# Kernel optimization log

Hardware: AMD Instinct MI355X
Metric: run time of the kernel (lower is better)

Reference implementation:

```python
import jax, jax.numpy as jnp
import numpy as np

B, N, C = 4, 2048, 1024
H = 16
D = C // H  # head_size = 64


def setup_inputs() -> dict:
    key = jax.random.key(0)
    ks = jax.random.split(key, 9)
    s = 1.0 / np.sqrt(C)
    return {
        "x": jax.random.normal(ks[0], (B, N, C), dtype=jnp.float32),
        "Wq": jax.random.normal(ks[1], (C, C), dtype=jnp.float32) * s,
        "bq": jnp.zeros((C,), dtype=jnp.float32),
        "Wk": jax.random.normal(ks[2], (C, C), dtype=jnp.float32) * s,
        "bk": jnp.zeros((C,), dtype=jnp.float32),
        "Wv": jax.random.normal(ks[3], (C, C), dtype=jnp.float32) * s,
        "bv": jnp.zeros((C,), dtype=jnp.float32),
        "Wo": jax.random.normal(ks[4], (C, C), dtype=jnp.float32) * s,
        "bo": jnp.zeros((C,), dtype=jnp.float32),
    }


def reference(x, Wq, bq, Wk, bk, Wv, bv, Wo, bo):
    scale = 1.0 / np.sqrt(D).astype(np.float32)
    # projections: [B,N,C] -> [B,H,N,D]
    def split_heads(t):
        return t.reshape(B, N, H, D).transpose(0, 2, 1, 3)
    q = split_heads(x @ Wq + bq)
    k = split_heads(x @ Wk + bk)
    v = split_heads(x @ Wv + bv)
    # scores: [B,H,N,N] -- full NxN materialized as in the original module
    attn = jnp.einsum("bhqd,bhkd->bhqk", q, k) * scale
    attn = jax.nn.softmax(attn, axis=-1)
    # context: [B,H,N,D] -> [B,N,C]
    ctx = jnp.einsum("bhqk,bhkd->bhqd", attn, v)
    ctx = ctx.transpose(0, 2, 1, 3).reshape(B, N, C)
    return ctx @ Wo + bo
```

## Files before the change

### kernel.cpp

```cpp
#include <hip/hip_runtime.h>
#include <hip/hip_bf16.h>

typedef __bf16 bf16_t;
typedef __bf16 bf16x4 __attribute__((ext_vector_type(4)));
typedef __bf16 bf16x8 __attribute__((ext_vector_type(8)));
typedef float f32x4 __attribute__((ext_vector_type(4)));
typedef unsigned int u32;

#define B_ 4
#define N_ 2048
#define C_ 1024
#define H_ 16
#define D_ 64

#define MFMA32(a, b, c) __builtin_amdgcn_mfma_f32_16x16x32_bf16((a), (b), (c), 0, 0, 0)

#if __has_builtin(__builtin_amdgcn_exp2f)
#define EXP2F(x) __builtin_amdgcn_exp2f(x)
#else
#define EXP2F(x) __expf((x) * 0.6931471805599453f)
#endif

#define QSCALE 0.18033688011112042f

__device__ __forceinline__ void async16(const bf16_t* g, bf16_t* l) {
    __builtin_amdgcn_global_load_lds(
        (const u32 __attribute__((address_space(1)))*)g,
        (u32 __attribute__((address_space(3)))*)l, 16, 0, 0);
}

__global__ __launch_bounds__(256)
void xconv_kernel(const float* __restrict__ x, bf16_t* __restrict__ xb)
{
    const size_t i = ((size_t)blockIdx.x * 256 + threadIdx.x) * 8;
    float4 a = *(const float4*)(x + i);
    float4 b = *(const float4*)(x + i + 4);
    bf16x8 o;
    o[0] = (bf16_t)a.x; o[1] = (bf16_t)a.y; o[2] = (bf16_t)a.z; o[3] = (bf16_t)a.w;
    o[4] = (bf16_t)b.x; o[5] = (bf16_t)b.y; o[6] = (bf16_t)b.z; o[7] = (bf16_t)b.w;
    *(bf16x8*)(xb + i) = o;
}

__global__ __launch_bounds__(256)
void wtrans_kernel(const float* __restrict__ W0, const float* __restrict__ W1,
                   const float* __restrict__ W2, const float* __restrict__ W3,
                   bf16_t* __restrict__ T0, bf16_t* __restrict__ T1,
                   bf16_t* __restrict__ T2, bf16_t* __restrict__ T3)
{
    const float* W; bf16_t* T;
    switch (blockIdx.z) {
        case 0:  W = W0; T = T0; break;
        case 1:  W = W1; T = T1; break;
        case 2:  W = W2; T = T2; break;
        default: W = W3; T = T3; break;
    }
    __shared__ bf16_t tile[64 * 72];
    const int tid = threadIdx.x;
    const int r0 = blockIdx.y * 64;
    const int c0 = blockIdx.x * 64;

    const int rr = tid >> 4;
    const int cc = (tid & 15) * 4;
    #pragma unroll
    for (int i = 0; i < 4; ++i) {
        const int row = rr + i * 16;
        float4 v = *(const float4*)(W + (size_t)(r0 + row) * C_ + c0 + cc);
        tile[(cc + 0) * 72 + row] = (bf16_t)v.x;
        tile[(cc + 1) * 72 + row] = (bf16_t)v.y;
        tile[(cc + 2) * 72 + row] = (bf16_t)v.z;
        tile[(cc + 3) * 72 + row] = (bf16_t)v.w;
    }
    __syncthreads();
    #pragma unroll
    for (int i = 0; i < 2; ++i) {
        const int ch = i * 256 + tid;
        const int n  = ch >> 3;
        const int k8 = (ch & 7) * 8;
        bf16x8 o = *(const bf16x8*)&tile[n * 72 + k8];
        *(bf16x8*)(T + (size_t)(c0 + n) * C_ + r0 + k8) = o;
    }
}

__global__ __launch_bounds__(256)
void gemm_qkv_kernel(const bf16_t* __restrict__ A, const bf16_t* __restrict__ Wt,
                     const float* __restrict__ bq, const float* __restrict__ bk,
                     const float* __restrict__ bv,
                     bf16_t* __restrict__ Qb, bf16_t* __restrict__ Kb,
                     bf16_t* __restrict__ Vtb)
{
    __shared__ bf16_t As[2][128 * 32];
    __shared__ bf16_t Bs[2][128 * 32];

    const int tid  = threadIdx.x;
    const int w    = tid >> 6;
    const int lane = tid & 63;
    const int c    = lane & 15;
    const int quad = lane >> 4;
    const int n0   = blockIdx.x * 128;
    const int m0   = blockIdx.y * 128;
    const int wm   = (w & 1) * 64;
    const int wn   = (w >> 1) * 64;

    f32x4 acc[4][4] = {};

    for (int k0 = 0; k0 < C_; k0 += 64) {
        __syncthreads();
        #pragma unroll
        for (int hh = 0; hh < 2; ++hh) {
            #pragma unroll
            for (int ph = 0; ph < 2; ++ph) {
                const int ch  = ph * 256 + tid;
                const int row = ch >> 2;
                const int k8  = (ch & 3) * 8;
                const int wbase = (ph * 256 + w * 64) * 8;
                async16(A  + (size_t)(m0 + row) * C_ + k0 + hh * 32 + k8, &As[hh][wbase]);
                async16(Wt + (size_t)(n0 + row) * C_ + k0 + hh * 32 + k8, &Bs[hh][wbase]);
            }
        }
        __syncthreads();

        bf16x8 af[2][4], bfr[2][4];
        #pragma unroll
        for (int hh = 0; hh < 2; ++hh) {
            #pragma unroll
            for (int mf = 0; mf < 4; ++mf)
                af[hh][mf] = *(const bf16x8*)&As[hh][(wm + mf * 16 + c) * 32 + quad * 8];
            #pragma unroll
            for (int nf = 0; nf < 4; ++nf)
                bfr[hh][nf] = *(const bf16x8*)&Bs[hh][(wn + nf * 16 + c) * 32 + quad * 8];
        }

        #pragma unroll
        for (int mf = 0; mf < 4; ++mf)
            #pragma unroll
            for (int nf = 0; nf < 4; ++nf) {
                acc[mf][nf] = MFMA32(af[0][mf], bfr[0][nf], acc[mf][nf]);
                acc[mf][nf] = MFMA32(af[1][mf], bfr[1][nf], acc[mf][nf]);
            }
    }

    const int which = n0 >> 10;
    const float* bias = (which == 0) ? bq : (which == 1) ? bk : bv;

    #pragma unroll
    for (int nf = 0; nf < 4; ++nf) {
        const int col  = n0 + wn + nf * 16 + c;
        const int ncol = col & 1023;
        const float bsf = bias[ncol];
        const int h = ncol >> 6, d = ncol & 63;
        #pragma unroll
        for (int mf = 0; mf < 4; ++mf) {
            const int rbase = m0 + wm + mf * 16 + quad * 4;
            if (which < 2) {
                bf16_t* out = which ? Kb : Qb;
                const float sc = which ? 1.0f : QSCALE;
                #pragma unroll
                for (int r = 0; r < 4; ++r) {
                    const int row = rbase + r;
                    const int bb = row >> 11, n = row & 2047;
                    out[(((size_t)bb * H_ + h) * N_ + n) * D_ + d] =
                        (bf16_t)((acc[mf][nf][r] + bsf) * sc);
                }
            } else {
                const int bb = rbase >> 11, nb = rbase & 2047;
                bf16x4 o;
                #pragma unroll
                for (int r = 0; r < 4; ++r) o[r] = (bf16_t)(acc[mf][nf][r] + bsf);
                *(bf16x4*)(Vtb + (((size_t)bb * H_ + h) * D_ + d) * N_ + nb) = o;
            }
        }
    }
}

__global__ __launch_bounds__(256)
void gemm_out_kernel(const bf16_t* __restrict__ A, const bf16_t* __restrict__ Bt,
                     const float* __restrict__ bias, float* __restrict__ out)
{
    __shared__ bf16_t As[2][128 * 32];
    __shared__ bf16_t Bs[2][128 * 32];

    const int tid  = threadIdx.x;
    const int w    = tid >> 6;
    const int lane = tid & 63;
    const int c    = lane & 15;
    const int quad = lane >> 4;
    const int n0   = blockIdx.x * 128;
    const int m0   = blockIdx.y * 128;
    const int wm   = (w & 1) * 64;
    const int wn   = (w >> 1) * 64;

    f32x4 acc[4][4] = {};

    for (int k0 = 0; k0 < C_; k0 += 64) {
        __syncthreads();
        #pragma unroll
        for (int hh = 0; hh < 2; ++hh) {
            #pragma unroll
            for (int ph = 0; ph < 2; ++ph) {
                const int ch  = ph * 256 + tid;
                const int row = ch >> 2;
                const int k8  = (ch & 3) * 8;
                const int wbase = (ph * 256 + w * 64) * 8;
                async16(A  + (size_t)(m0 + row) * C_ + k0 + hh * 32 + k8, &As[hh][wbase]);
                async16(Bt + (size_t)(n0 + row) * C_ + k0 + hh * 32 + k8, &Bs[hh][wbase]);
            }
        }
        __syncthreads();

        bf16x8 af[2][4], bfr[2][4];
        #pragma unroll
        for (int hh = 0; hh < 2; ++hh) {
            #pragma unroll
            for (int mf = 0; mf < 4; ++mf)
                af[hh][mf] = *(const bf16x8*)&As[hh][(wm + mf * 16 + c) * 32 + quad * 8];
            #pragma unroll
            for (int nf = 0; nf < 4; ++nf)
                bfr[hh][nf] = *(const bf16x8*)&Bs[hh][(wn + nf * 16 + c) * 32 + quad * 8];
        }

        #pragma unroll
        for (int mf = 0; mf < 4; ++mf)
            #pragma unroll
            for (int nf = 0; nf < 4; ++nf) {
                acc[mf][nf] = MFMA32(af[0][mf], bfr[0][nf], acc[mf][nf]);
                acc[mf][nf] = MFMA32(af[1][mf], bfr[1][nf], acc[mf][nf]);
            }
    }

    #pragma unroll
    for (int nf = 0; nf < 4; ++nf) {
        const int col   = n0 + wn + nf * 16 + c;
        const float bsf = bias[col];
        #pragma unroll
        for (int mf = 0; mf < 4; ++mf) {
            const int rbase = m0 + wm + mf * 16 + quad * 4;
            #pragma unroll
            for (int r = 0; r < 4; ++r)
                out[(size_t)(rbase + r) * C_ + col] = acc[mf][nf][r] + bsf;
        }
    }
}

__global__ __launch_bounds__(256, 2)
void attn_kernel(const bf16_t* __restrict__ Q, const bf16_t* __restrict__ K,
                 const bf16_t* __restrict__ Vt, bf16_t* __restrict__ ctx)
{
    __shared__ bf16_t ksh[64 * 64];
    __shared__ bf16_t vsh[64 * 64];

    const int tid  = threadIdx.x;
    const int w    = tid >> 6;
    const int lane = tid & 63;
    const int c    = lane & 15;
    const int quad = lane >> 4;

    const int bid   = blockIdx.x;
    const int bh    = (bid & 7) * 8 + ((bid >> 3) & 7);
    const int qtile = bid >> 6;
    const int b = bh >> 4, h = bh & 15;
    const size_t base = (size_t)bh * N_ * D_;
    const int qb = qtile * 256 + w * 64;

    bf16x8 qf[4][2];
    #pragma unroll
    for (int g = 0; g < 4; ++g)
        #pragma unroll
        for (int hh = 0; hh < 2; ++hh)
            qf[g][hh] = *(const bf16x8*)(Q + base + (size_t)(qb + g * 16 + c) * D_ + hh * 32 + quad * 8);

    bf16x8 ones;
    #pragma unroll
    for (int j = 0; j < 8; ++j) ones[j] = (bf16_t)1.0f;

    f32x4 O[4][4] = {};
    f32x4 O5[4] = {};

    for (int kt = 0; kt < N_; kt += 64) {
        __syncthreads();
        #pragma unroll
        for (int ph = 0; ph < 2; ++ph) {
            const int ch = ph * 256 + tid;
            const int rr = ch >> 3;
            const int e8 = ch & 7;
            const int sw = (e8 ^ (rr & 7)) * 8;
            bf16x8 kv = *(const bf16x8*)(K  + base + (size_t)(kt + rr) * D_ + e8 * 8);
            *(bf16x8*)&ksh[rr * 64 + sw] = kv;
            bf16x8 vv = *(const bf16x8*)(Vt + base + (size_t)rr * N_ + kt + e8 * 8);
            *(bf16x8*)&vsh[rr * 64 + sw] = vv;
        }
        __syncthreads();

        #pragma unroll
        for (int ss = 0; ss < 2; ++ss) {
            bf16x8 kb[2][2];
            #pragma unroll
            for (int s2 = 0; s2 < 2; ++s2) {
                const int key = (ss * 2 + s2) * 16 + c;
                #pragma unroll
                for (int hh = 0; hh < 2; ++hh)
                    kb[s2][hh] = *(const bf16x8*)&ksh[key * 64 + (((hh * 4 + quad) ^ (c & 7)) * 8)];
            }
            bf16x8 va[4];
            const int k8lo = ss * 4 + (quad >> 1);
            const int half = (quad & 1) * 4;
            #pragma unroll
            for (int df = 0; df < 4; ++df) {
                const int row = (df * 16 + c) * 64;
                bf16x4 lo = *(const bf16x4*)&vsh[row + ((k8lo       ^ (c & 7)) * 8) + half];
                bf16x4 hi = *(const bf16x4*)&vsh[row + (((k8lo + 2) ^ (c & 7)) * 8) + half];
                #pragma unroll
                for (int j = 0; j < 4; ++j) { va[df][j] = lo[j]; va[df][4 + j] = hi[j]; }
            }

            #pragma unroll
            for (int g = 0; g < 4; ++g) {
                f32x4 s0 = {}, s1 = {};
                s0 = MFMA32(kb[0][0], qf[g][0], s0);
                s0 = MFMA32(kb[0][1], qf[g][1], s0);
                s1 = MFMA32(kb[1][0], qf[g][0], s1);
                s1 = MFMA32(kb[1][1], qf[g][1], s1);

                bf16x8 pb;
                #pragma unroll
                for (int r = 0; r < 4; ++r) {
                    pb[r]     = (bf16_t)EXP2F(s0[r]);
                    pb[4 + r] = (bf16_t)EXP2F(s1[r]);
                }

                #pragma unroll
                for (int df = 0; df < 4; ++df)
                    O[g][df] = MFMA32(va[df], pb, O[g][df]);
                O5[g] = MFMA32(ones, pb, O5[g]);
            }
        }
    }

    #pragma unroll
    for (int g = 0; g < 4; ++g) {
        const float inv_l = 1.0f / O5[g][0];
        const int q = qb + g * 16 + c;
        #pragma unroll
        for (int df = 0; df < 4; ++df) {
            bf16x4 o;
            #pragma unroll
            for (int r = 0; r < 4; ++r) o[r] = (bf16_t)(O[g][df][r] * inv_l);
            *(bf16x4*)(ctx + ((size_t)b * N_ + q) * C_ + h * 64 + df * 16 + quad * 4) = o;
        }
    }
}

extern "C" void kernel_launch(void* const* d_in, const int* in_sizes, int n_in,
                              void* d_out, int out_size, void* d_ws, size_t ws_size,
                              hipStream_t stream) {
    const float* x  = (const float*)d_in[0];
    const float* Wq = (const float*)d_in[1];
    const float* bq = (const float*)d_in[2];
    const float* Wk = (const float*)d_in[3];
    const float* bk = (const float*)d_in[4];
    const float* Wv = (const float*)d_in[5];
    const float* bv = (const float*)d_in[6];
    const float* Wo = (const float*)d_in[7];
    const float* bo = (const float*)d_in[8];

    bf16_t* ws = (bf16_t*)d_ws;
    const size_t per = (size_t)B_ * N_ * C_;
    bf16_t* xb  = ws;
    bf16_t* ctx = ws;
    bf16_t* Qb  = ws + per;
    bf16_t* Kb  = ws + 2 * per;
    bf16_t* Vtb = ws + 3 * per;
    bf16_t* Wtqkv = ws + 4 * per;
    bf16_t* Wtq = Wtqkv;
    bf16_t* Wtk = Wtqkv + (size_t)C_ * C_;
    bf16_t* Wtv = Wtqkv + 2 * (size_t)C_ * C_;
    bf16_t* Wto = Wtqkv + 3 * (size_t)C_ * C_;

    dim3 blk(256);

    xconv_kernel<<<dim3(per / 2048), blk, 0, stream>>>(x, xb);
    wtrans_kernel<<<dim3(16, 16, 4), blk, 0, stream>>>(Wq, Wk, Wv, Wo, Wtq, Wtk, Wtv, Wto);

    gemm_qkv_kernel<<<dim3(24, 64), blk, 0, stream>>>(xb, Wtqkv, bq, bk, bv, Qb, Kb, Vtb);

    attn_kernel<<<dim3(512), blk, 0, stream>>>(Qb, Kb, Vtb, ctx);

    gemm_out_kernel<<<dim3(8, 64), blk, 0, stream>>>(ctx, Wto, bo, (float*)d_out);
}
```

Baseline: 270.8 us.

## Restructure QKV GEMM into 256x256 double-buffered pipelined tiles with swizzled LDS

```diff
diff --git a/kernel.cpp b/kernel.cpp
--- a/kernel.cpp
+++ b/kernel.cpp
@@ -28,6 +28,12 @@
         (const u32 __attribute__((address_space(1)))*)g,
         (u32 __attribute__((address_space(3)))*)l, 16, 0, 0);
 }
+
+#define SBAR()  asm volatile("s_barrier" ::: "memory")
+#define LGKM0() do { asm volatile("s_waitcnt lgkmcnt(0)" ::: "memory"); \
+                     __builtin_amdgcn_sched_barrier(0); } while (0)
+#define VM4()   asm volatile("s_waitcnt vmcnt(4)" ::: "memory")
+#define VM0()   asm volatile("s_waitcnt vmcnt(0)" ::: "memory")
 
 __global__ __launch_bounds__(256)
 void xconv_kernel(const float* __restrict__ x, bf16_t* __restrict__ xb)
@@ -81,62 +87,129 @@
     }
 }
 
-__global__ __launch_bounds__(256)
+#define NT_ 16
+
+__device__ __forceinline__ void ld4(const bf16_t* slab, int rbase, int c, int quad,
+                                    bf16x8 (&dst)[4])
+{
+    #pragma unroll
+    for (int i = 0; i < 4; ++i) {
+        const int row = rbase + i * 16 + c;
+        dst[i] = *(const bf16x8*)(slab + row * 32 + ((quad ^ (row & 3)) * 8));
+    }
+}
+
+__device__ __forceinline__ void mfma16(f32x4 (&acc)[8][4], const bf16x8 (&af)[4],
+                                       const bf16x8 (&bfv)[4], int mf0)
+{
+    #pragma unroll
+    for (int i = 0; i < 4; ++i)
+        #pragma unroll
+        for (int j = 0; j < 4; ++j)
+            acc[mf0 + i][j] = MFMA32(af[i], bfv[j], acc[mf0 + i][j]);
+}
+
+__device__ __forceinline__ void stage2(const bf16_t* p0, const bf16_t* p1,
+                                       bf16_t* slab, int koff, int dstoff)
+{
+    async16(p0 + koff, slab + dstoff);
+    async16(p1 + koff, slab + 4096 + dstoff);
+}
+
+__global__ __launch_bounds__(512, 2)
 void gemm_qkv_kernel(const bf16_t* __restrict__ A, const bf16_t* __restrict__ Wt,
                      const float* __restrict__ bq, const float* __restrict__ bk,
                      const float* __restrict__ bv,
                      bf16_t* __restrict__ Qb, bf16_t* __restrict__ Kb,
                      bf16_t* __restrict__ Vtb)
 {
-    __shared__ bf16_t As[2][128 * 32];
-    __shared__ bf16_t Bs[2][128 * 32];
+    __shared__ bf16_t Asm[2][2][256 * 32];
+    __shared__ bf16_t Bsm[2][2][256 * 32];
 
     const int tid  = threadIdx.x;
     const int w    = tid >> 6;
     const int lane = tid & 63;
     const int c    = lane & 15;
     const int quad = lane >> 4;
-    const int n0   = blockIdx.x * 128;
-    const int m0   = blockIdx.y * 128;
-    const int wm   = (w & 1) * 64;
-    const int wn   = (w >> 1) * 64;
-
-    f32x4 acc[4][4] = {};
-
-    for (int k0 = 0; k0 < C_; k0 += 64) {
-        __syncthreads();
-        #pragma unroll
-        for (int hh = 0; hh < 2; ++hh) {
-            #pragma unroll
-            for (int ph = 0; ph < 2; ++ph) {
-                const int ch  = ph * 256 + tid;
-                const int row = ch >> 2;
-                const int k8  = (ch & 3) * 8;
-                const int wbase = (ph * 256 + w * 64) * 8;
-                async16(A  + (size_t)(m0 + row) * C_ + k0 + hh * 32 + k8, &As[hh][wbase]);
-                async16(Wt + (size_t)(n0 + row) * C_ + k0 + hh * 32 + k8, &Bs[hh][wbase]);
-            }
-        }
-        __syncthreads();
-
-        bf16x8 af[2][4], bfr[2][4];
-        #pragma unroll
-        for (int hh = 0; hh < 2; ++hh) {
-            #pragma unroll
-            for (int mf = 0; mf < 4; ++mf)
-                af[hh][mf] = *(const bf16x8*)&As[hh][(wm + mf * 16 + c) * 32 + quad * 8];
-            #pragma unroll
-            for (int nf = 0; nf < 4; ++nf)
-                bfr[hh][nf] = *(const bf16x8*)&Bs[hh][(wn + nf * 16 + c) * 32 + quad * 8];
-        }
-
-        #pragma unroll
-        for (int mf = 0; mf < 4; ++mf)
-            #pragma unroll
-            for (int nf = 0; nf < 4; ++nf) {
-                acc[mf][nf] = MFMA32(af[0][mf], bfr[0][nf], acc[mf][nf]);
-                acc[mf][nf] = MFMA32(af[1][mf], bfr[1][nf], acc[mf][nf]);
-            }
+    const int wr   = w >> 2;
+    const int wc   = w & 3;
+
+    const int bid = blockIdx.x;
+    const int swz = (bid & 7) * 48 + (bid >> 3);
+    const int mb  = swz & 31, nb = swz >> 5;
+    const int m0  = mb * 256, n0 = nb * 256;
+
+    const int ci0 = tid,       r0s = ci0 >> 2, kc0 = (ci0 & 3) ^ (r0s & 3);
+    const int ci1 = tid + 512, r1s = ci1 >> 2, kc1 = (ci1 & 3) ^ (r1s & 3);
+    const bf16_t* Ast0 = A  + (size_t)(m0 + r0s) * C_ + kc0 * 8;
+    const bf16_t* Ast1 = A  + (size_t)(m0 + r1s) * C_ + kc1 * 8;
+    const bf16_t* Bst0 = Wt + (size_t)(n0 + r0s) * C_ + kc0 * 8;
+    const bf16_t* Bst1 = Wt + (size_t)(n0 + r1s) * C_ + kc1 * 8;
+    const int dstoff = w * 512;
+
+    f32x4 acc[8][4] = {};
+    bf16x8 af[4], bfv[4];
+
+    stage2(Ast0, Ast1, &Asm[0][0][0], 0,  dstoff);
+    stage2(Bst0, Bst1, &Bsm[0][0][0], 0,  dstoff);
+    stage2(Ast0, Ast1, &Asm[0][1][0], 32, dstoff);
+    stage2(Bst0, Bst1, &Bsm[0][1][0], 32, dstoff);
+    VM4();
+    SBAR();
+
+    #pragma unroll 2
+    for (int t = 0; t < NT_; ++t) {
+        const int  cur  = t & 1;
+        const bool more = (t + 1) < NT_;
+        const int  kn   = (t + 1) << 6;
+        const bf16_t* A0 = &Asm[cur][0][0];
+        const bf16_t* A1 = &Asm[cur][1][0];
+        const bf16_t* B0 = &Bsm[cur][0][0];
+        const bf16_t* B1 = &Bsm[cur][1][0];
+        bf16_t* nA0 = &Asm[cur ^ 1][0][0];
+        bf16_t* nA1 = &Asm[cur ^ 1][1][0];
+        bf16_t* nB0 = &Bsm[cur ^ 1][0][0];
+        bf16_t* nB1 = &Bsm[cur ^ 1][1][0];
+
+        ld4(A0, wr * 128,      c, quad, af);
+        ld4(B0, wc * 64,       c, quad, bfv);
+        if (more) stage2(Ast0, Ast1, nA0, kn, dstoff);
+        SBAR();
+        LGKM0();
+        __builtin_amdgcn_s_setprio(1);
+        mfma16(acc, af, bfv, 0);
+        __builtin_amdgcn_s_setprio(0);
+        SBAR();
+
+        ld4(A0, wr * 128 + 64, c, quad, af);
+        if (more) stage2(Bst0, Bst1, nB0, kn, dstoff);
+        SBAR();
+        LGKM0();
+        __builtin_amdgcn_s_setprio(1);
+        mfma16(acc, af, bfv, 4);
+        __builtin_amdgcn_s_setprio(0);
+        if (more) VM4(); else VM0();
+        SBAR();
+
+        ld4(A1, wr * 128 + 64, c, quad, af);
+        ld4(B1, wc * 64,       c, quad, bfv);
+        if (more) stage2(Ast0, Ast1, nA1, kn + 32, dstoff);
+        SBAR();
+        LGKM0();
+        __builtin_amdgcn_s_setprio(1);
+        mfma16(acc, af, bfv, 4);
+        __builtin_amdgcn_s_setprio(0);
+        SBAR();
+
+        ld4(A1, wr * 128,      c, quad, af);
+        if (more) stage2(Bst0, Bst1, nB1, kn + 32, dstoff);
+        SBAR();
+        LGKM0();
+        __builtin_amdgcn_s_setprio(1);
+        mfma16(acc, af, bfv, 0);
+        __builtin_amdgcn_s_setprio(0);
+        if (more) VM4();
+        SBAR();
     }
 
     const int which = n0 >> 10;
@@ -144,13 +217,13 @@
 
     #pragma unroll
     for (int nf = 0; nf < 4; ++nf) {
-        const int col  = n0 + wn + nf * 16 + c;
+        const int col  = n0 + wc * 64 + nf * 16 + c;
         const int ncol = col & 1023;
         const float bsf = bias[ncol];
         const int h = ncol >> 6, d = ncol & 63;
         #pragma unroll
-        for (int mf = 0; mf < 4; ++mf) {
-            const int rbase = m0 + wm + mf * 16 + quad * 4;
+        for (int mf = 0; mf < 8; ++mf) {
+            const int rbase = m0 + wr * 128 + mf * 16 + quad * 4;
             if (which < 2) {
                 bf16_t* out = which ? Kb : Qb;
                 const float sc = which ? 1.0f : QSCALE;
@@ -162,11 +235,11 @@
                         (bf16_t)((acc[mf][nf][r] + bsf) * sc);
                 }
             } else {
-                const int bb = rbase >> 11, nb = rbase & 2047;
+                const int bb = rbase >> 11, nbv = rbase & 2047;
                 bf16x4 o;
                 #pragma unroll
                 for (int r = 0; r < 4; ++r) o[r] = (bf16_t)(acc[mf][nf][r] + bsf);
-                *(bf16x4*)(Vtb + (((size_t)bb * H_ + h) * D_ + d) * N_ + nb) = o;
+                *(bf16x4*)(Vtb + (((size_t)bb * H_ + h) * D_ + d) * N_ + nbv) = o;
             }
         }
     }
@@ -380,7 +453,7 @@
     xconv_kernel<<<dim3(per / 2048), blk, 0, stream>>>(x, xb);
     wtrans_kernel<<<dim3(16, 16, 4), blk, 0, stream>>>(Wq, Wk, Wv, Wo, Wtq, Wtk, Wtv, Wto);
 
-    gemm_qkv_kernel<<<dim3(24, 64), blk, 0, stream>>>(xb, Wtqkv, bq, bk, bv, Qb, Kb, Vtb);
+    gemm_qkv_kernel<<<dim3(384), dim3(512), 0, stream>>>(xb, Wtqkv, bq, bk, bv, Qb, Kb, Vtb);
 
     attn_kernel<<<dim3(512), blk, 0, stream>>>(Qb, Kb, Vtb, ctx);
 
```

Result: slower. 278.9 us (+3.0%).

## Rewrite QKV GEMM as 256x256 double-buffered pipelined kernel with swizzled LDS

Applied to the files above, without the earlier changes.

```diff
diff --git a/kernel.cpp b/kernel.cpp
--- a/kernel.cpp
+++ b/kernel.cpp
@@ -28,6 +28,10 @@
         (const u32 __attribute__((address_space(1)))*)g,
         (u32 __attribute__((address_space(3)))*)l, 16, 0, 0);
 }
+
+#define SBAR()  asm volatile("s_barrier" ::: "memory")
+#define VM4()   asm volatile("s_waitcnt vmcnt(4)" ::: "memory")
+#define VM0()   asm volatile("s_waitcnt vmcnt(0)" ::: "memory")
 
 __global__ __launch_bounds__(256)
 void xconv_kernel(const float* __restrict__ x, bf16_t* __restrict__ xb)
@@ -81,76 +85,131 @@
     }
 }
 
-__global__ __launch_bounds__(256)
+
+__device__ __forceinline__ void mfma16(f32x4 (&acc)[8][4], const bf16x8 (&af)[4],
+                                       const bf16x8 (&bfv)[4], int mf0)
+{
+    #pragma unroll
+    for (int i = 0; i < 4; ++i)
+        #pragma unroll
+        for (int j = 0; j < 4; ++j)
+            acc[mf0 + i][j] = MFMA32(af[i], bfv[j], acc[mf0 + i][j]);
+}
+
+__global__ __launch_bounds__(512) __attribute__((amdgpu_waves_per_eu(2, 2)))
 void gemm_qkv_kernel(const bf16_t* __restrict__ A, const bf16_t* __restrict__ Wt,
                      const float* __restrict__ bq, const float* __restrict__ bk,
                      const float* __restrict__ bv,
                      bf16_t* __restrict__ Qb, bf16_t* __restrict__ Kb,
                      bf16_t* __restrict__ Vtb)
 {
-    __shared__ bf16_t As[2][128 * 32];
-    __shared__ bf16_t Bs[2][128 * 32];
+    __shared__ bf16_t smem[65536];
 
     const int tid  = threadIdx.x;
     const int w    = tid >> 6;
     const int lane = tid & 63;
     const int c    = lane & 15;
     const int quad = lane >> 4;
-    const int n0   = blockIdx.x * 128;
-    const int m0   = blockIdx.y * 128;
-    const int wm   = (w & 1) * 64;
-    const int wn   = (w >> 1) * 64;
-
-    f32x4 acc[4][4] = {};
-
-    for (int k0 = 0; k0 < C_; k0 += 64) {
-        __syncthreads();
-        #pragma unroll
-        for (int hh = 0; hh < 2; ++hh) {
-            #pragma unroll
-            for (int ph = 0; ph < 2; ++ph) {
-                const int ch  = ph * 256 + tid;
-                const int row = ch >> 2;
-                const int k8  = (ch & 3) * 8;
-                const int wbase = (ph * 256 + w * 64) * 8;
-                async16(A  + (size_t)(m0 + row) * C_ + k0 + hh * 32 + k8, &As[hh][wbase]);
-                async16(Wt + (size_t)(n0 + row) * C_ + k0 + hh * 32 + k8, &Bs[hh][wbase]);
-            }
-        }
-        __syncthreads();
-
-        bf16x8 af[2][4], bfr[2][4];
-        #pragma unroll
-        for (int hh = 0; hh < 2; ++hh) {
-            #pragma unroll
-            for (int mf = 0; mf < 4; ++mf)
-                af[hh][mf] = *(const bf16x8*)&As[hh][(wm + mf * 16 + c) * 32 + quad * 8];
-            #pragma unroll
-            for (int nf = 0; nf < 4; ++nf)
-                bfr[hh][nf] = *(const bf16x8*)&Bs[hh][(wn + nf * 16 + c) * 32 + quad * 8];
-        }
-
-        #pragma unroll
-        for (int mf = 0; mf < 4; ++mf)
-            #pragma unroll
-            for (int nf = 0; nf < 4; ++nf) {
-                acc[mf][nf] = MFMA32(af[0][mf], bfr[0][nf], acc[mf][nf]);
-                acc[mf][nf] = MFMA32(af[1][mf], bfr[1][nf], acc[mf][nf]);
-            }
-    }
+    const int wr   = w >> 2;
+    const int wc   = w & 3;
+
+    const int bid = blockIdx.x;
+    const int x8  = bid & 7;
+    const int ii  = bid >> 3;
+    const int mb  = x8 * 4 + (ii & 3);
+    const int nb  = ii >> 2;
+    const int m0  = mb * 256, n0 = nb * 256;
+
+    const int r0s = tid >> 2;
+    const int kc  = (tid & 3) ^ (r0s & 3);
+    const bf16_t* Ast0 = A  + (size_t)(m0 + r0s) * C_ + kc * 8;
+    const bf16_t* Ast1 = A  + (size_t)(m0 + r0s + 128) * C_ + kc * 8;
+    const bf16_t* Bst0 = Wt + (size_t)(n0 + r0s) * C_ + kc * 8;
+    const bf16_t* Bst1 = Wt + (size_t)(n0 + r0s + 128) * C_ + kc * 8;
+
+    const int xorc = (quad ^ (c & 3)) * 8;
+    const bf16_t* Ard = smem + (wr * 128 + c) * 32 + xorc;
+    const bf16_t* Brd = smem + 32768 + (wc * 64 + c) * 32 + xorc;
+    bf16_t* sAB = smem + w * 512;
+
+#define STAGE_A(BUF, KS, KOFF) do { \
+    async16(Ast0 + (KOFF), sAB + (BUF) * 16384 + (KS) * 8192); \
+    async16(Ast1 + (KOFF), sAB + (BUF) * 16384 + (KS) * 8192 + 4096); } while (0)
+#define STAGE_B(BUF, KS, KOFF) do { \
+    async16(Bst0 + (KOFF), sAB + 32768 + (BUF) * 16384 + (KS) * 8192); \
+    async16(Bst1 + (KOFF), sAB + 32768 + (BUF) * 16384 + (KS) * 8192 + 4096); } while (0)
+#define LD4A(BUF, KS, HALF) do { \
+    af[0] = *(const bf16x8*)(Ard + (BUF) * 16384 + (KS) * 8192 + (HALF) * 2048); \
+    af[1] = *(const bf16x8*)(Ard + (BUF) * 16384 + (KS) * 8192 + (HALF) * 2048 + 512); \
+    af[2] = *(const bf16x8*)(Ard + (BUF) * 16384 + (KS) * 8192 + (HALF) * 2048 + 1024); \
+    af[3] = *(const bf16x8*)(Ard + (BUF) * 16384 + (KS) * 8192 + (HALF) * 2048 + 1536); } while (0)
+#define LD4B(BUF, KS) do { \
+    bfv[0] = *(const bf16x8*)(Brd + (BUF) * 16384 + (KS) * 8192); \
+    bfv[1] = *(const bf16x8*)(Brd + (BUF) * 16384 + (KS) * 8192 + 512); \
+    bfv[2] = *(const bf16x8*)(Brd + (BUF) * 16384 + (KS) * 8192 + 1024); \
+    bfv[3] = *(const bf16x8*)(Brd + (BUF) * 16384 + (KS) * 8192 + 1536); } while (0)
+
+#define TILE(CUR, DOSTAGE) do { \
+    LD4A(CUR, 0, 0); LD4B(CUR, 0); \
+    if (DOSTAGE) STAGE_A(1 - (CUR), 0, 64); \
+    SBAR(); \
+    __builtin_amdgcn_s_setprio(1); mfma16(acc, af, bfv, 0); __builtin_amdgcn_s_setprio(0); \
+    SBAR(); \
+    LD4A(CUR, 0, 1); \
+    if (DOSTAGE) STAGE_B(1 - (CUR), 0, 64); \
+    SBAR(); \
+    __builtin_amdgcn_s_setprio(1); mfma16(acc, af, bfv, 4); __builtin_amdgcn_s_setprio(0); \
+    if (DOSTAGE) VM4(); else VM0(); \
+    SBAR(); \
+    LD4A(CUR, 1, 1); LD4B(CUR, 1); \
+    if (DOSTAGE) STAGE_A(1 - (CUR), 1, 96); \
+    SBAR(); \
+    __builtin_amdgcn_s_setprio(1); mfma16(acc, af, bfv, 4); __builtin_amdgcn_s_setprio(0); \
+    SBAR(); \
+    LD4A(CUR, 1, 0); \
+    if (DOSTAGE) STAGE_B(1 - (CUR), 1, 96); \
+    SBAR(); \
+    __builtin_amdgcn_s_setprio(1); mfma16(acc, af, bfv, 0); __builtin_amdgcn_s_setprio(0); \
+    if (DOSTAGE) { VM4(); Ast0 += 64; Ast1 += 64; Bst0 += 64; Bst1 += 64; } \
+    SBAR(); \
+} while (0)
+
+    f32x4 acc[8][4] = {};
+    bf16x8 af[4], bfv[4];
+
+    STAGE_A(0, 0, 0);
+    STAGE_B(0, 0, 0);
+    STAGE_A(0, 1, 32);
+    STAGE_B(0, 1, 32);
+    VM4();
+    SBAR();
+
+    #pragma unroll 1
+    for (int tt = 0; tt < 7; ++tt) {
+        TILE(0, 1);
+        TILE(1, 1);
+    }
+    TILE(0, 1);
+    TILE(1, 0);
+
+#undef TILE
+#undef LD4A
+#undef LD4B
+#undef STAGE_A
+#undef STAGE_B
 
     const int which = n0 >> 10;
     const float* bias = (which == 0) ? bq : (which == 1) ? bk : bv;
 
     #pragma unroll
     for (int nf = 0; nf < 4; ++nf) {
-        const int col  = n0 + wn + nf * 16 + c;
+        const int col  = n0 + wc * 64 + nf * 16 + c;
         const int ncol = col & 1023;
         const float bsf = bias[ncol];
         const int h = ncol >> 6, d = ncol & 63;
         #pragma unroll
-        for (int mf = 0; mf < 4; ++mf) {
-            const int rbase = m0 + wm + mf * 16 + quad * 4;
+        for (int mf = 0; mf < 8; ++mf) {
+            const int rbase = m0 + wr * 128 + mf * 16 + quad * 4;
             if (which < 2) {
                 bf16_t* out = which ? Kb : Qb;
                 const float sc = which ? 1.0f : QSCALE;
@@ -162,11 +221,11 @@
                         (bf16_t)((acc[mf][nf][r] + bsf) * sc);
                 }
             } else {
-                const int bb = rbase >> 11, nb = rbase & 2047;
+                const int bb = rbase >> 11, nbv = rbase & 2047;
                 bf16x4 o;
                 #pragma unroll
                 for (int r = 0; r < 4; ++r) o[r] = (bf16_t)(acc[mf][nf][r] + bsf);
-                *(bf16x4*)(Vtb + (((size_t)bb * H_ + h) * D_ + d) * N_ + nb) = o;
+                *(bf16x4*)(Vtb + (((size_t)bb * H_ + h) * D_ + d) * N_ + nbv) = o;
             }
         }
     }
@@ -380,7 +439,7 @@
     xconv_kernel<<<dim3(per / 2048), blk, 0, stream>>>(x, xb);
     wtrans_kernel<<<dim3(16, 16, 4), blk, 0, stream>>>(Wq, Wk, Wv, Wo, Wtq, Wtk, Wtv, Wto);
 
-    gemm_qkv_kernel<<<dim3(24, 64), blk, 0, stream>>>(xb, Wtqkv, bq, bk, bv, Qb, Kb, Vtb);
+    gemm_qkv_kernel<<<dim3(384), dim3(512), 0, stream>>>(xb, Wtqkv, bq, bk, bv, Qb, Kb, Vtb);
 
     attn_kernel<<<dim3(512), blk, 0, stream>>>(Qb, Kb, Vtb, ctx);
 
```

Measured after the change: 273.9 us. No clear change (+1.1%).
